# Kernel optimization log

Measured on AMD Instinct MI355X. Metric: run time of the kernel, lower is better.

Reference implementation:

```python
import jax, jax.numpy as jnp
import numpy as np

LEVEL = 20            # module default -> 21 max-pool passes, kernels 1x1 .. 41x41 (H,W only)
K_SIG = 10.0          # init arg k: sigmoid weight sharpness
N_POOL = LEVEL + 1    # len(max_pool)
DENOM = N_POOL + 1    # torch: level = len(max_pool) + 1 = 22


def _edge3d(mask):
    # Equivalent to F.conv3d(mask, filt, padding=1) > 0 where filt is the
    # in-plane Laplacian: center 1, 4 H/W-neighbors -0.25, zeros elsewhere.
    p = jnp.pad(mask, ((0, 0), (0, 0), (0, 0), (1, 1), (1, 1)))
    lap = mask - 0.25 * (p[..., :-2, 1:-1] + p[..., 2:, 1:-1]
                         + p[..., 1:-1, :-2] + p[..., 1:-1, 2:])
    return (lap > 0).astype(jnp.float32)


def _mp3(x):
    # stride-1 3x3 max pool over H,W with same padding (pads with -inf like torch MaxPool)
    return jax.lax.reduce_window(x, -jnp.inf, jax.lax.max,
                                 (1, 1, 1, 3, 3), (1, 1, 1, 1, 1),
                                 ((0, 0), (0, 0), (0, 0), (1, 1), (1, 1)))


def _cal_dist(mask):
    edge = _edge3d(mask)  # [B,1,D,H,W] binary
    # maxpool with window (2k+1)x(2k+1) on a binary map == k cascaded 3x3 dilations,
    # so sum_{k=0}^{LEVEL} maxpool_{2k+1}(edge) is computed incrementally.
    def body(i, carry):
        e, acc = carry
        return (_mp3(e), acc + e)
    _, acc = jax.lax.fori_loop(0, N_POOL, body, (edge, jnp.zeros_like(edge)))
    return (DENOM - acc) / DENOM


def setup_inputs() -> dict:
    key = jax.random.key(0)
    k1, k2 = jax.random.split(key)
    outputs = jax.random.uniform(k1, (2, 1, 64, 256, 256), dtype=jnp.float32)
    masks = jax.random.randint(k2, (2, 1, 64, 256, 256), 0, 2, dtype=jnp.int32)
    return {"outputs": outputs, "masks": masks}


def reference(outputs, masks):
    eps = 1e-6
    m = masks.astype(jnp.float32)
    dist = _cal_dist(m)
    weight = jax.lax.stop_gradient(2.0 / (1.0 + jnp.exp(K_SIG * dist)))
    b = outputs.shape[0]
    ow = (outputs.astype(jnp.float32) * weight).reshape(b, -1)
    mw = (m * weight).reshape(b, -1)
    intersect = jnp.sum(ow * m.reshape(b, -1), axis=1)
    input_area = jnp.sum(ow, axis=1)
    target_area = jnp.sum(mw, axis=1)
    batch_loss = 1.0 - 2.0 * intersect / (input_area + target_area + 2.0 * eps)
    batch_loss = jnp.where(target_area == 0, 0.0, batch_loss)
    return batch_loss.mean()
```

## Files before the change

### kernel.cpp

```cpp
#include <hip/hip_runtime.h>
#include <stdint.h>

typedef unsigned long long u64;

#define SLICES 128
#define WPS 1024
#define TOTAL_WORDS (SLICES * WPS)
#define NBLK3 1024


__global__ __launch_bounds__(256) void k_packdilate(const int* __restrict__ masks,
                                                    u64* __restrict__ mbits,
                                                    u64* __restrict__ planes) {
    __shared__ u64 rows[256][5];
    __shared__ u64 tmp[256][5];

    const int t = threadIdx.x;
    const int slice = blockIdx.x;

    u64 m[4];
    const int4* src = (const int4*)(masks + (size_t)slice * 65536 + t * 256);
    #pragma unroll
    for (int j = 0; j < 4; ++j) {
        u64 w = 0ull;
        #pragma unroll
        for (int g = 0; g < 16; ++g) {
            int4 v = src[j * 16 + g];
            w |= (u64)(v.x != 0) << (g * 4 + 0);
            w |= (u64)(v.y != 0) << (g * 4 + 1);
            w |= (u64)(v.z != 0) << (g * 4 + 2);
            w |= (u64)(v.w != 0) << (g * 4 + 3);
        }
        m[j] = w;
        rows[t][j] = w;
        mbits[(size_t)slice * WPS + t * 4 + j] = w;
    }
    __syncthreads();

    u64 c[4];
    {
        u64 up[4], dn[4];
        #pragma unroll
        for (int j = 0; j < 4; ++j) {
            up[j] = (t > 0)   ? rows[t - 1][j] : 0ull;
            dn[j] = (t < 255) ? rows[t + 1][j] : 0ull;
        }
        #pragma unroll
        for (int j = 0; j < 4; ++j) {
            u64 lf = (m[j] << 1) | (j > 0 ? (m[j - 1] >> 63) : 0ull);
            u64 rt = (m[j] >> 1) | (j < 3 ? (m[j + 1] << 63) : 0ull);
            c[j] = m[j] & ~(up[j] & dn[j] & lf & rt);
        }
    }

    u64 p[5][4];
    #pragma unroll
    for (int pl = 0; pl < 5; ++pl)
        #pragma unroll
        for (int j = 0; j < 4; ++j) p[pl][j] = 0ull;


    for (int k = 1; k <= 20; ++k) {
        u64 h[4];
        #pragma unroll
        for (int j = 0; j < 4; ++j) {
            u64 lf = (c[j] << 1) | (j > 0 ? (c[j - 1] >> 63) : 0ull);
            u64 rt = (c[j] >> 1) | (j < 3 ? (c[j + 1] << 63) : 0ull);
            h[j] = c[j] | lf | rt;
            tmp[t][j] = h[j];
        }
        __syncthreads();
        #pragma unroll
        for (int j = 0; j < 4; ++j) {
            u64 u_ = (t > 0)   ? tmp[t - 1][j] : 0ull;
            u64 d_ = (t < 255) ? tmp[t + 1][j] : 0ull;
            u64 n = h[j] | u_ | d_;
            u64 nw = n & ~c[j];
            c[j] = n;
            #pragma unroll
            for (int pl = 0; pl < 5; ++pl)
                if ((k >> pl) & 1) p[pl][j] |= nw;
        }
        int done = ((c[0] & c[1] & c[2] & c[3]) == 0xFFFFFFFFFFFFFFFFull) ? 1 : 0;
        if (__syncthreads_and(done)) break;
    }

    #pragma unroll
    for (int j = 0; j < 4; ++j) {
        u64 u_ = ~c[j];
        p[0][j] |= u_; p[2][j] |= u_; p[4][j] |= u_;
    }

    #pragma unroll
    for (int pl = 0; pl < 5; ++pl)
        #pragma unroll
        for (int j = 0; j < 4; ++j)
            planes[(size_t)pl * TOTAL_WORDS + (size_t)slice * WPS + t * 4 + j] = p[pl][j];
}

__global__ __launch_bounds__(256) void k_reduce(const float* __restrict__ outputs,
                                               const u64* __restrict__ mbits,
                                               const u64* __restrict__ planes,
                                               float* __restrict__ partials) {
    __shared__ float wtab[22];
    __shared__ float red[4][6];
    const int t = threadIdx.x;
    if (t < 22) wtab[t] = 2.0f / (1.0f + __expf(10.0f * (float)(t + 1) * (1.0f / 22.0f)));
    __syncthreads();

    const int tid = blockIdx.x * 256 + t;
    float s[2][3];
    #pragma unroll
    for (int b = 0; b < 2; ++b) { s[b][0] = s[b][1] = s[b][2] = 0.0f; }

    #pragma unroll
    for (int b = 0; b < 2; ++b) {
        for (int i = 0; i < 4; ++i) {
            int pix4 = b * 1048576 + i * 262144 + tid;
            int pix = pix4 * 4;
            float4 o4 = ((const float4*)outputs)[pix4];
            float ov[4] = {o4.x, o4.y, o4.z, o4.w};
            int widx = pix >> 6;
            int sh = pix & 63;
            u64 mw = mbits[widx];
            u64 p0 = planes[widx];
            u64 p1 = planes[TOTAL_WORDS + widx];
            u64 p2 = planes[2 * TOTAL_WORDS + widx];
            u64 p3 = planes[3 * TOTAL_WORDS + widx];
            u64 p4 = planes[4 * TOTAL_WORDS + widx];
            #pragma unroll
            for (int q = 0; q < 4; ++q) {
                int s2 = sh + q;
                int d0 = (int)((p0 >> s2) & 1ull)
                       | ((int)((p1 >> s2) & 1ull) << 1)
                       | ((int)((p2 >> s2) & 1ull) << 2)
                       | ((int)((p3 >> s2) & 1ull) << 3)
                       | ((int)((p4 >> s2) & 1ull) << 4);
                float w = wtab[d0];
                float ow = ov[q] * w;
                s[b][0] += ow;
                if ((mw >> s2) & 1ull) { s[b][1] += w; s[b][2] += ow; }
            }
        }
    }

    #pragma unroll
    for (int b = 0; b < 2; ++b)
        #pragma unroll
        for (int k = 0; k < 3; ++k) {
            float v = s[b][k];
            #pragma unroll
            for (int off = 32; off > 0; off >>= 1) v += __shfl_down(v, off);
            s[b][k] = v;
        }
    const int lane = t & 63, wv = t >> 6;
    if (lane == 0) {
        #pragma unroll
        for (int b = 0; b < 2; ++b)
            #pragma unroll
            for (int k = 0; k < 3; ++k) red[wv][b * 3 + k] = s[b][k];
    }
    __syncthreads();
    if (t < 6) {
        float v = red[0][t] + red[1][t] + red[2][t] + red[3][t];
        partials[blockIdx.x * 6 + t] = v;
    }
}

__global__ __launch_bounds__(64) void k_fin(const float* __restrict__ partials,
                                            float* __restrict__ out) {
    const int lane = threadIdx.x;
    float s[6] = {0, 0, 0, 0, 0, 0};
    for (int i = lane; i < NBLK3; i += 64)
        #pragma unroll
        for (int k = 0; k < 6; ++k) s[k] += partials[i * 6 + k];
    #pragma unroll
    for (int k = 0; k < 6; ++k) {
        float v = s[k];
        #pragma unroll
        for (int off = 32; off > 0; off >>= 1) v += __shfl_down(v, off);
        s[k] = v;
    }
    if (lane == 0) {
        float loss = 0.0f;
        #pragma unroll
        for (int b = 0; b < 2; ++b) {
            float A = s[b * 3 + 0];
            float T = s[b * 3 + 1];
            float I = s[b * 3 + 2];
            float l = (T == 0.0f) ? 0.0f : (1.0f - 2.0f * I / (A + T + 2e-6f));
            loss += l;
        }
        out[0] = 0.5f * loss;
    }
}

extern "C" void kernel_launch(void* const* d_in, const int* in_sizes, int n_in,
                              void* d_out, int out_size, void* d_ws, size_t ws_size,
                              hipStream_t stream) {
    const float* outputs = (const float*)d_in[0];
    const int* masks = (const int*)d_in[1];
    float* out = (float*)d_out;

    u64* mbits = (u64*)d_ws;
    u64* planes = mbits + TOTAL_WORDS;
    float* partials = (float*)((char*)d_ws + (size_t)6 * TOTAL_WORDS * 8);

    k_packdilate<<<SLICES, 256, 0, stream>>>(masks, mbits, planes);
    k_reduce<<<NBLK3, 256, 0, stream>>>(outputs, mbits, planes, partials);
    k_fin<<<1, 64, 0, stream>>>(partials, out);
}
```

Measured before the change: 113.2 us.

## Pack mask bits with wave ballots and fold final reduction into last block

The mask packing now has each wavefront read 64 consecutive ints per step with coalesced loads and build the bit word via __ballot, staged in shared memory. Before, each thread read 256 strided ints as int4 and shifted bits itself. The separate finalize kernel is removed: the last reduce block, found with an atomic counter plus threadfence, sums the partials and writes the loss. The intent is better coalescing on the 32 MB mask read and one less kernel launch. The cost is an atomic and an extra shared buffer, and the counter reset relies on the earlier kernel.

```diff
diff --git a/kernel.cpp b/kernel.cpp
--- a/kernel.cpp
+++ b/kernel.cpp
@@ -11,29 +11,35 @@
 
 __global__ __launch_bounds__(256) void k_packdilate(const int* __restrict__ masks,
                                                     u64* __restrict__ mbits,
-                                                    u64* __restrict__ planes) {
+                                                    u64* __restrict__ planes,
+                                                    unsigned* __restrict__ counter) {
+    __shared__ u64 packed[WPS];
     __shared__ u64 rows[256][5];
     __shared__ u64 tmp[256][5];
 
     const int t = threadIdx.x;
     const int slice = blockIdx.x;
+    if (slice == 0 && t == 0) *counter = 0u;
+
+    {
+        const int wv = t >> 6, lane = t & 63;
+        const int* base = masks + (size_t)slice * 65536;
+        #pragma unroll 4
+        for (int i = 0; i < 256; ++i) {
+            int w = (wv << 8) + i;
+            int v = base[(w << 6) + lane];
+            u64 bal = __ballot(v != 0);
+            if (lane == 0) packed[w] = bal;
+        }
+    }
+    __syncthreads();
 
     u64 m[4];
-    const int4* src = (const int4*)(masks + (size_t)slice * 65536 + t * 256);
     #pragma unroll
     for (int j = 0; j < 4; ++j) {
-        u64 w = 0ull;
-        #pragma unroll
-        for (int g = 0; g < 16; ++g) {
-            int4 v = src[j * 16 + g];
-            w |= (u64)(v.x != 0) << (g * 4 + 0);
-            w |= (u64)(v.y != 0) << (g * 4 + 1);
-            w |= (u64)(v.z != 0) << (g * 4 + 2);
-            w |= (u64)(v.w != 0) << (g * 4 + 3);
-        }
-        m[j] = w;
-        rows[t][j] = w;
-        mbits[(size_t)slice * WPS + t * 4 + j] = w;
+        m[j] = packed[t * 4 + j];
+        rows[t][j] = m[j];
+        mbits[(size_t)slice * WPS + t * 4 + j] = m[j];
     }
     __syncthreads();
 
@@ -101,9 +107,12 @@
 __global__ __launch_bounds__(256) void k_reduce(const float* __restrict__ outputs,
                                                const u64* __restrict__ mbits,
                                                const u64* __restrict__ planes,
-                                               float* __restrict__ partials) {
+                                               float* __restrict__ partials,
+                                               unsigned* __restrict__ counter,
+                                               float* __restrict__ out) {
     __shared__ float wtab[22];
     __shared__ float red[4][6];
+    __shared__ int sLast;
     const int t = threadIdx.x;
     if (t < 22) wtab[t] = 2.0f / (1.0f + __expf(10.0f * (float)(t + 1) * (1.0f / 22.0f)));
     __syncthreads();
@@ -165,33 +174,40 @@
         float v = red[0][t] + red[1][t] + red[2][t] + red[3][t];
         partials[blockIdx.x * 6 + t] = v;
     }
-}
-
-__global__ __launch_bounds__(64) void k_fin(const float* __restrict__ partials,
-                                            float* __restrict__ out) {
-    const int lane = threadIdx.x;
-    float s[6] = {0, 0, 0, 0, 0, 0};
-    for (int i = lane; i < NBLK3; i += 64)
-        #pragma unroll
-        for (int k = 0; k < 6; ++k) s[k] += partials[i * 6 + k];
-    #pragma unroll
-    for (int k = 0; k < 6; ++k) {
-        float v = s[k];
-        #pragma unroll
-        for (int off = 32; off > 0; off >>= 1) v += __shfl_down(v, off);
-        s[k] = v;
-    }
-    if (lane == 0) {
-        float loss = 0.0f;
-        #pragma unroll
-        for (int b = 0; b < 2; ++b) {
-            float A = s[b * 3 + 0];
-            float T = s[b * 3 + 1];
-            float I = s[b * 3 + 2];
-            float l = (T == 0.0f) ? 0.0f : (1.0f - 2.0f * I / (A + T + 2e-6f));
-            loss += l;
-        }
-        out[0] = 0.5f * loss;
+    __syncthreads();
+    if (t == 0) {
+        __threadfence();
+        unsigned old = atomicAdd(counter, 1u);
+        sLast = (old == (unsigned)(NBLK3 - 1)) ? 1 : 0;
+    }
+    __syncthreads();
+    if (sLast) {
+        __threadfence();
+        if (t < 64) {
+            float sf[6] = {0, 0, 0, 0, 0, 0};
+            for (int i = t; i < NBLK3; i += 64)
+                #pragma unroll
+                for (int k = 0; k < 6; ++k) sf[k] += partials[i * 6 + k];
+            #pragma unroll
+            for (int k = 0; k < 6; ++k) {
+                float v = sf[k];
+                #pragma unroll
+                for (int off = 32; off > 0; off >>= 1) v += __shfl_down(v, off);
+                sf[k] = v;
+            }
+            if (t == 0) {
+                float loss = 0.0f;
+                #pragma unroll
+                for (int b = 0; b < 2; ++b) {
+                    float A = sf[b * 3 + 0];
+                    float T = sf[b * 3 + 1];
+                    float I = sf[b * 3 + 2];
+                    float l = (T == 0.0f) ? 0.0f : (1.0f - 2.0f * I / (A + T + 2e-6f));
+                    loss += l;
+                }
+                out[0] = 0.5f * loss;
+            }
+        }
     }
 }
 
@@ -205,8 +221,8 @@
     u64* mbits = (u64*)d_ws;
     u64* planes = mbits + TOTAL_WORDS;
     float* partials = (float*)((char*)d_ws + (size_t)6 * TOTAL_WORDS * 8);
-
-    k_packdilate<<<SLICES, 256, 0, stream>>>(masks, mbits, planes);
-    k_reduce<<<NBLK3, 256, 0, stream>>>(outputs, mbits, planes, partials);
-    k_fin<<<1, 64, 0, stream>>>(partials, out);
+    unsigned* counter = (unsigned*)(partials + NBLK3 * 6);
+
+    k_packdilate<<<SLICES, 256, 0, stream>>>(masks, mbits, planes, counter);
+    k_reduce<<<NBLK3, 256, 0, stream>>>(outputs, mbits, planes, partials, counter, out);
 }
```

New measurement: 201.4 us. +77.9%, slower.
